# Kernel optimization log

Hardware: AMD Instinct MI355X
Metric: run time of the kernel (lower is better)

Reference implementation:

```python
import jax, jax.numpy as jnp
import numpy as np

B, T, D = 32, 2048, 512


def setup_inputs() -> dict:
    key = jax.random.key(0)
    x = jax.random.normal(key, (B, T, D), dtype=jnp.float32)
    return {"x": x}


def reference(x):
    """DmvCell RNN with aggregations ('mean','var','max').

    Active partials: count, sum, max, mean, sn (Welford M2), var.
    Per step t:
        count += 1
        sum   += x_t
        max    = maximum(max, x_t)
        prev_mean = mean; mean = sum / count
        sn    += (x_t - prev_mean) * (x_t - mean)
        var    = sn / count
        out_t  = concat([mean, var, max])
    Initial states are zeros (Keras default). Returns the full output
    sequence [B, T, 3*D].
    """
    b, t, d = x.shape
    dt = x.dtype

    def step(carry, xt):
        count, s, mx, mean, sn = carry
        count = count + jnp.asarray(1, dt)          # [B,1]
        s = s + xt                                   # [B,D]
        mx = jnp.maximum(mx, xt)                     # [B,D]
        prev_mean = mean
        mean = s / count                             # [B,D]
        sn = sn + (xt - prev_mean) * (xt - mean)     # [B,D]
        var = sn / count                             # [B,D]
        out = jnp.concatenate([mean, var, mx], axis=-1)  # [B,3D]
        return (count, s, mx, mean, sn), out

    init = (
        jnp.zeros((b, 1), dt),   # count
        jnp.zeros((b, d), dt),   # sum
        jnp.zeros((b, d), dt),   # max
        jnp.zeros((b, d), dt),   # mean
        jnp.zeros((b, d), dt),   # sn
    )
    _, ys = jax.lax.scan(step, init, jnp.swapaxes(x, 0, 1))  # ys: [T,B,3D]
    return jnp.swapaxes(ys, 0, 1)  # [B,T,3D]
```

## Files before the change

### kernel.cpp

```cpp
#include <hip/hip_runtime.h>


#define BB 32
#define TT 2048
#define DD 512
#define DGRP 64
#define NW 16
#define CHUNK (TT / NW)

__device__ __forceinline__ float fast_rcp(float x) {
#if __has_builtin(__builtin_amdgcn_rcpf)
    return __builtin_amdgcn_rcpf(x);
#else
    return 1.0f / x;
#endif
}

__launch_bounds__(1024, 1)
__global__ void dmv_scan_kernel(const float* __restrict__ x,
                                float* __restrict__ out) {
    __shared__ float aggS[NW][DGRP];
    __shared__ float aggM2[NW][DGRP];
    __shared__ float aggMX[NW][DGRP];

    const int tid = threadIdx.x;
    const int w   = tid >> 6;
    const int l   = tid & 63;
    const int b   = blockIdx.x >> 3;
    const int d0  = (blockIdx.x & 7) * DGRP;

    const float* xp = x   + ((size_t)b * TT) * DD + d0 + l
                          + (size_t)(w * CHUNK) * DD;
    float*       op = out + ((size_t)b * TT) * (3 * DD) + d0 + l
                          + (size_t)(w * CHUNK) * (3 * DD);

    if (w < NW - 1) {
        float s = 0.f, ss = 0.f, mx = 0.f;
        #pragma unroll 8
        for (int k = 0; k < CHUNK; ++k) {
            float xv = xp[(size_t)k * DD];
            s  += xv;
            ss  = fmaf(xv, xv, ss);
            mx  = fmaxf(mx, xv);
        }
        aggS[w][l]  = s;
        aggM2[w][l] = ss - s * s * (1.0f / CHUNK);
        aggMX[w][l] = mx;
    }
    __syncthreads();

    float c_n = 0.f, c_s = 0.f, c_m2 = 0.f, c_mx = 0.f;
    for (int j = 0; j < w; ++j) {
        float bs = aggS[j][l], bm2 = aggM2[j][l], bmx = aggMX[j][l];
        if (j == 0) {
            c_n = (float)CHUNK; c_s = bs; c_m2 = bm2; c_mx = bmx;
        } else {
            float n  = c_n + (float)CHUNK;
            float da = bs * (1.0f / CHUNK) - c_s / c_n;
            c_m2 = c_m2 + bm2 + da * da * (c_n * (float)CHUNK / n);
            c_s += bs;
            c_mx = fmaxf(c_mx, bmx);
            c_n  = n;
        }
    }

    float cnt   = c_n;
    float rs    = c_s, rm2 = c_m2, rmx = c_mx;
    float rmean = (w > 0) ? rs / cnt : 0.f;
    #pragma unroll 8
    for (int k = 0; k < CHUNK; ++k) {
        float xv = xp[(size_t)k * DD];
        cnt += 1.f;
        float inv = fast_rcp(cnt);
        rs  += xv;
        rmx  = fmaxf(rmx, xv);
        float nm = rs * inv;
        rm2 += (xv - rmean) * (xv - nm);
        rmean = nm;
        float var = rm2 * inv;
        float* orow = op + (size_t)k * (3 * DD);
        orow[0]      = nm;
        orow[DD]     = var;
        orow[2 * DD] = rmx;
    }
}

extern "C" void kernel_launch(void* const* d_in, const int* in_sizes, int n_in,
                              void* d_out, int out_size, void* d_ws, size_t ws_size,
                              hipStream_t stream) {
    (void)in_sizes; (void)n_in; (void)d_ws; (void)ws_size; (void)out_size;
    const float* x = (const float*)d_in[0];
    float* out = (float*)d_out;
    dim3 grid(BB * (DD / DGRP));
    dim3 block(1024);
    dmv_scan_kernel<<<grid, block, 0, stream>>>(x, out);
}
```

Measured before the change: 139.4 us.

## Split scan into aggregate, prefix and scan kernels over global workspace with float4

Replaces the single-kernel block-local chunked scan with three kernels: per-chunk aggregation into a global workspace, a per-chain exclusive prefix combine, and a final chunked scan that writes outputs. This lets the time dimension be split into up to 64 chunks across the whole grid instead of 16 per block, and uses float4 loads and stores. In exchange it adds workspace traffic, two extra launches, and depends on the workspace size, falling back to the old kernel when the workspace is too small.

Measured after the change: 152.7 us. +9.5%, slower.

```diff
diff --git a/kernel.cpp b/kernel.cpp
--- a/kernel.cpp
+++ b/kernel.cpp
@@ -4,9 +4,8 @@
 #define BB 32
 #define TT 2048
 #define DD 512
-#define DGRP 64
-#define NW 16
-#define CHUNK (TT / NW)
+#define NF4 ((BB * DD) / 4)
+#define NCHAIN (BB * DD)
 
 __device__ __forceinline__ float fast_rcp(float x) {
 #if __has_builtin(__builtin_amdgcn_rcpf)
@@ -16,12 +15,143 @@
 #endif
 }
 
+template <int NW>
+__launch_bounds__(256)
+__global__ void dmv_agg_kernel(const float* __restrict__ x,
+                               float4* __restrict__ ws) {
+    constexpr int CHUNK = TT / NW;
+    float4* __restrict__ aS  = ws;
+    float4* __restrict__ aM2 = ws + (size_t)NW * NF4;
+    float4* __restrict__ aMX = ws + 2 * (size_t)NW * NF4;
+
+    const int tid = blockIdx.x * 256 + threadIdx.x;
+    const int W   = tid >> 6;
+    const int l   = tid & 63;
+    const int col = W & 63;
+    const int c   = W >> 6;
+    const int b   = col >> 1, h = col & 1;
+    const int chain = col * 64 + l;
+
+    const float* xp = x + ((size_t)b * TT + (size_t)c * CHUNK) * DD
+                        + h * 256 + l * 4;
+
+    float s[4]  = {0.f, 0.f, 0.f, 0.f};
+    float ss[4] = {0.f, 0.f, 0.f, 0.f};
+    float mx[4] = {0.f, 0.f, 0.f, 0.f};
+    #pragma unroll 8
+    for (int k = 0; k < CHUNK; ++k) {
+        float4 xv = *(const float4*)(xp + (size_t)k * DD);
+        float v[4] = {xv.x, xv.y, xv.z, xv.w};
+        #pragma unroll
+        for (int j = 0; j < 4; ++j) {
+            s[j]  += v[j];
+            ss[j]  = fmaf(v[j], v[j], ss[j]);
+            mx[j]  = fmaxf(mx[j], v[j]);
+        }
+    }
+    const size_t o = (size_t)c * NF4 + chain;
+    aS[o]  = make_float4(s[0], s[1], s[2], s[3]);
+    aM2[o] = make_float4(ss[0] - s[0] * s[0] * (1.f / CHUNK),
+                         ss[1] - s[1] * s[1] * (1.f / CHUNK),
+                         ss[2] - s[2] * s[2] * (1.f / CHUNK),
+                         ss[3] - s[3] * s[3] * (1.f / CHUNK));
+    aMX[o] = make_float4(mx[0], mx[1], mx[2], mx[3]);
+}
+
+template <int NW>
+__launch_bounds__(256)
+__global__ void dmv_prefix_kernel(float* __restrict__ ws) {
+    constexpr int CHUNK = TT / NW;
+    float* __restrict__ aS  = ws;
+    float* __restrict__ aM2 = ws + (size_t)NW * NCHAIN;
+    float* __restrict__ aMX = ws + 2 * (size_t)NW * NCHAIN;
+
+    const size_t i = (size_t)blockIdx.x * 256 + threadIdx.x;
+
+    float rs = aS[i], rm2 = aM2[i], rmx = aMX[i];
+    aS[i] = 0.f; aM2[i] = 0.f; aMX[i] = 0.f;
+    float rn = (float)CHUNK;
+    #pragma unroll 8
+    for (int c = 1; c < NW; ++c) {
+        const size_t idx = (size_t)c * NCHAIN + i;
+        float ts = aS[idx], tm2 = aM2[idx], tmx = aMX[idx];
+        aS[idx] = rs; aM2[idx] = rm2; aMX[idx] = rmx;
+        float n  = rn + (float)CHUNK;
+        float da = ts * (1.f / CHUNK) - rs / rn;
+        rm2 = rm2 + tm2 + da * da * (rn * (float)CHUNK / n);
+        rs += ts;
+        rmx = fmaxf(rmx, tmx);
+        rn  = n;
+    }
+}
+
+template <int NW>
+__launch_bounds__(256)
+__global__ void dmv_scan_kernel2(const float* __restrict__ x,
+                                 const float4* __restrict__ ws,
+                                 float* __restrict__ out) {
+    constexpr int CHUNK = TT / NW;
+    const float4* __restrict__ aS  = ws;
+    const float4* __restrict__ aM2 = ws + (size_t)NW * NF4;
+    const float4* __restrict__ aMX = ws + 2 * (size_t)NW * NF4;
+
+    const int tid = blockIdx.x * 256 + threadIdx.x;
+    const int W   = tid >> 6;
+    const int l   = tid & 63;
+    const int col = W & 63;
+    const int c   = W >> 6;
+    const int b   = col >> 1, h = col & 1;
+    const int chain = col * 64 + l;
+
+    const size_t o = (size_t)c * NF4 + chain;
+    float4 cS = aS[o], cM2 = aM2[o], cMX = aMX[o];
+
+    float rs[4]    = {cS.x, cS.y, cS.z, cS.w};
+    float rm2[4]   = {cM2.x, cM2.y, cM2.z, cM2.w};
+    float rmx[4]   = {cMX.x, cMX.y, cMX.z, cMX.w};
+    float rmean[4];
+    float cnt = (float)(c * CHUNK);
+    #pragma unroll
+    for (int j = 0; j < 4; ++j) rmean[j] = (c > 0) ? rs[j] / cnt : 0.f;
+
+    const float* xp = x + ((size_t)b * TT + (size_t)c * CHUNK) * DD
+                        + h * 256 + l * 4;
+    float* op = out + ((size_t)b * TT + (size_t)c * CHUNK) * (3 * DD)
+                    + h * 256 + l * 4;
+
+    #pragma unroll 8
+    for (int k = 0; k < CHUNK; ++k) {
+        float4 xv = *(const float4*)(xp + (size_t)k * DD);
+        float v[4] = {xv.x, xv.y, xv.z, xv.w};
+        cnt += 1.f;
+        float inv = fast_rcp(cnt);
+        float var[4];
+        #pragma unroll
+        for (int j = 0; j < 4; ++j) {
+            rs[j] += v[j];
+            rmx[j] = fmaxf(rmx[j], v[j]);
+            float nm = rs[j] * inv;
+            rm2[j] += (v[j] - rmean[j]) * (v[j] - nm);
+            rmean[j] = nm;
+            var[j] = rm2[j] * inv;
+        }
+        float* row = op + (size_t)k * (3 * DD);
+        *(float4*)(row)          = make_float4(rmean[0], rmean[1], rmean[2], rmean[3]);
+        *(float4*)(row + DD)     = make_float4(var[0], var[1], var[2], var[3]);
+        *(float4*)(row + 2 * DD) = make_float4(rmx[0], rmx[1], rmx[2], rmx[3]);
+    }
+}
+
+#define FNW 16
+#define FCHUNK (TT / FNW)
+#define DGRP 64
+
 __launch_bounds__(1024, 1)
-__global__ void dmv_scan_kernel(const float* __restrict__ x,
-                                float* __restrict__ out) {
-    __shared__ float aggS[NW][DGRP];
-    __shared__ float aggM2[NW][DGRP];
-    __shared__ float aggMX[NW][DGRP];
+__global__ void dmv_scan_fallback(const float* __restrict__ x,
+                                  float* __restrict__ out) {
+    __shared__ float aggS[FNW][DGRP];
+    __shared__ float aggM2[FNW][DGRP];
+    __shared__ float aggMX[FNW][DGRP];
 
     const int tid = threadIdx.x;
     const int w   = tid >> 6;
@@ -30,21 +160,19 @@
     const int d0  = (blockIdx.x & 7) * DGRP;
 
     const float* xp = x   + ((size_t)b * TT) * DD + d0 + l
-                          + (size_t)(w * CHUNK) * DD;
+                          + (size_t)(w * FCHUNK) * DD;
     float*       op = out + ((size_t)b * TT) * (3 * DD) + d0 + l
-                          + (size_t)(w * CHUNK) * (3 * DD);
-
-    if (w < NW - 1) {
+                          + (size_t)(w * FCHUNK) * (3 * DD);
+
+    if (w < FNW - 1) {
         float s = 0.f, ss = 0.f, mx = 0.f;
         #pragma unroll 8
-        for (int k = 0; k < CHUNK; ++k) {
+        for (int k = 0; k < FCHUNK; ++k) {
             float xv = xp[(size_t)k * DD];
-            s  += xv;
-            ss  = fmaf(xv, xv, ss);
-            mx  = fmaxf(mx, xv);
-        }
-        aggS[w][l]  = s;
-        aggM2[w][l] = ss - s * s * (1.0f / CHUNK);
+            s += xv; ss = fmaf(xv, xv, ss); mx = fmaxf(mx, xv);
+        }
+        aggS[w][l] = s;
+        aggM2[w][l] = ss - s * s * (1.0f / FCHUNK);
         aggMX[w][l] = mx;
     }
     __syncthreads();
@@ -53,45 +181,59 @@
     for (int j = 0; j < w; ++j) {
         float bs = aggS[j][l], bm2 = aggM2[j][l], bmx = aggMX[j][l];
         if (j == 0) {
-            c_n = (float)CHUNK; c_s = bs; c_m2 = bm2; c_mx = bmx;
+            c_n = (float)FCHUNK; c_s = bs; c_m2 = bm2; c_mx = bmx;
         } else {
-            float n  = c_n + (float)CHUNK;
-            float da = bs * (1.0f / CHUNK) - c_s / c_n;
-            c_m2 = c_m2 + bm2 + da * da * (c_n * (float)CHUNK / n);
-            c_s += bs;
-            c_mx = fmaxf(c_mx, bmx);
-            c_n  = n;
-        }
-    }
-
-    float cnt   = c_n;
-    float rs    = c_s, rm2 = c_m2, rmx = c_mx;
+            float n  = c_n + (float)FCHUNK;
+            float da = bs * (1.0f / FCHUNK) - c_s / c_n;
+            c_m2 = c_m2 + bm2 + da * da * (c_n * (float)FCHUNK / n);
+            c_s += bs; c_mx = fmaxf(c_mx, bmx); c_n = n;
+        }
+    }
+
+    float cnt = c_n, rs = c_s, rm2 = c_m2, rmx = c_mx;
     float rmean = (w > 0) ? rs / cnt : 0.f;
     #pragma unroll 8
-    for (int k = 0; k < CHUNK; ++k) {
+    for (int k = 0; k < FCHUNK; ++k) {
         float xv = xp[(size_t)k * DD];
         cnt += 1.f;
         float inv = fast_rcp(cnt);
-        rs  += xv;
-        rmx  = fmaxf(rmx, xv);
+        rs += xv; rmx = fmaxf(rmx, xv);
         float nm = rs * inv;
         rm2 += (xv - rmean) * (xv - nm);
         rmean = nm;
         float var = rm2 * inv;
         float* orow = op + (size_t)k * (3 * DD);
-        orow[0]      = nm;
-        orow[DD]     = var;
-        orow[2 * DD] = rmx;
-    }
+        orow[0] = nm; orow[DD] = var; orow[2 * DD] = rmx;
+    }
+}
+
+template <int NW>
+static void launch_3k(const float* x, float* out, void* d_ws, hipStream_t stream) {
+    float4* ws4 = (float4*)d_ws;
+    dim3 blk(256);
+    dmv_agg_kernel<NW><<<dim3(16 * NW), blk, 0, stream>>>(x, ws4);
+    dmv_prefix_kernel<NW><<<dim3(NCHAIN / 256), blk, 0, stream>>>((float*)d_ws);
+    dmv_scan_kernel2<NW><<<dim3(16 * NW), blk, 0, stream>>>(x, ws4, out);
 }
 
 extern "C" void kernel_launch(void* const* d_in, const int* in_sizes, int n_in,
                               void* d_out, int out_size, void* d_ws, size_t ws_size,
                               hipStream_t stream) {
-    (void)in_sizes; (void)n_in; (void)d_ws; (void)ws_size; (void)out_size;
+    (void)in_sizes; (void)n_in; (void)out_size;
     const float* x = (const float*)d_in[0];
     float* out = (float*)d_out;
-    dim3 grid(BB * (DD / DGRP));
-    dim3 block(1024);
-    dmv_scan_kernel<<<grid, block, 0, stream>>>(x, out);
-}
+
+    const size_t need64 = (size_t)3 * 64 * NF4 * sizeof(float4);
+    const size_t need32 = (size_t)3 * 32 * NF4 * sizeof(float4);
+    const size_t need16 = (size_t)3 * 16 * NF4 * sizeof(float4);
+
+    if (d_ws && ws_size >= need64) {
+        launch_3k<64>(x, out, d_ws, stream);
+    } else if (d_ws && ws_size >= need32) {
+        launch_3k<32>(x, out, d_ws, stream);
+    } else if (d_ws && ws_size >= need16) {
+        launch_3k<16>(x, out, d_ws, stream);
+    } else {
+        dmv_scan_fallback<<<dim3(BB * (DD / DGRP)), dim3(1024), 0, stream>>>(x, out);
+    }
+}
```
